# Performance work log

Hardware: AMD Instinct MI355X
Metric: run time of the kernel (lower is better)

Reference implementation:

```python
import jax, jax.numpy as jnp
import numpy as np
import math

PHI = (1 + math.sqrt(5)) / 2
VOCAB = 50257
EMBED_DIM = 1024
NUM_WINDINGS = 8
EPS = 1e-5


def _generate_coprimes(n):
    coprimes = [1, 2]
    while len(coprimes) < n:
        nxt = int(coprimes[-1] * PHI) + 1
        while any(math.gcd(nxt, c) > 1 for c in coprimes):
            nxt += 1
        coprimes.append(nxt)
    return coprimes[:n]


def setup_inputs() -> dict:
    key = jax.random.key(0)
    k1, k2, k3 = jax.random.split(key, 3)
    B, S = 8, 4096
    x = jax.random.randint(k1, (B, S), 0, VOCAB, dtype=jnp.int64)
    windings = jnp.asarray(_generate_coprimes(NUM_WINDINGS), dtype=jnp.float32)
    win_dim = 2 * NUM_WINDINGS
    # nn.Linear default init: U(-1/sqrt(fan_in), 1/sqrt(fan_in))
    bound = 1.0 / math.sqrt(win_dim)
    proj_w = jax.random.uniform(k2, (EMBED_DIM, win_dim), jnp.float32, -bound, bound)
    proj_b = jax.random.uniform(k3, (EMBED_DIM,), jnp.float32, -bound, bound)
    gamma = jnp.ones((EMBED_DIM,), jnp.float32)
    beta = jnp.zeros((EMBED_DIM,), jnp.float32)
    return {"x": x, "windings": windings, "proj_w": proj_w, "proj_b": proj_b,
            "gamma": gamma, "beta": beta}


def reference(x, windings, proj_w, proj_b, gamma, beta):
    # t in [0,1): fractional position on the torus
    t = x.astype(jnp.float32) / VOCAB                      # (B, S)
    angle = (2.0 * jnp.pi) * t[..., None] * windings       # (B, S, W)
    # torch loop appends cos, sin per winding -> interleaved [cos0,sin0,cos1,sin1,...]
    feats = jnp.stack([jnp.cos(angle), jnp.sin(angle)], axis=-1)  # (B, S, W, 2)
    feats = feats.reshape(*angle.shape[:-1], 2 * windings.shape[0])  # (B, S, 2W)
    emb = jnp.einsum('bsf,df->bsd', feats, proj_w) + proj_b  # (B, S, D)
    # SyntonicNorm: LayerNorm-style normalization over embed_dim with affine params
    mu = jnp.mean(emb, axis=-1, keepdims=True)
    var = jnp.mean(jnp.square(emb - mu), axis=-1, keepdims=True)
    normed = (emb - mu) * jax.lax.rsqrt(var + EPS)
    return normed * gamma + beta
```

## Files before the change

### kernel.cpp

```cpp
#include <hip/hip_runtime.h>
#include <math.h>


#define TWO_PI 6.28318530717958647692f
#define INV_VOCAB (1.0f / 50257.0f)
#define INV_D (1.0f / 1024.0f)
#define ROWS_PB 64
#define PSTRIDE 320
#define FINAL_OFF 20480

typedef float f32x4 __attribute__((ext_vector_type(4)));

__global__ __launch_bounds__(256) void stats_partial(const float* __restrict__ pw,
                                                     const float* __restrict__ pb,
                                                     float* __restrict__ ws) {
  const int t = threadIdx.x;
  const int b = blockIdx.x;
  const int f = t >> 4, g = t & 15;
  const int d0 = b * 16;

  float m = 0.f, mw = 0.f, cc = 0.f, b1 = 0.f, b2 = 0.f;
#pragma unroll
  for (int k = 0; k < 16; ++k) {
    const int d = d0 + k;
    const float wf = pw[d * 16 + f];
    const float wg = pw[d * 16 + g];
    m = fmaf(wf, wg, m);
    if (g == 0) {
      const float bb = pb[d];
      mw += wf;
      cc = fmaf(wf, bb, cc);
      if (f == 0) {
        b1 += bb;
        b2 = fmaf(bb, bb, b2);
      }
    }
  }
  float* p = ws + b * PSTRIDE;
  p[t] = m * INV_D;
  if (g == 0) {
    p[256 + f] = mw * INV_D;
    p[272 + f] = cc * INV_D;
    if (f == 0) {
      p[288] = b1 * INV_D;
      p[289] = b2 * INV_D;
    }
  }
}

__global__ __launch_bounds__(320) void stats_reduce(float* __restrict__ ws) {
  const int t = threadIdx.x;
  float s = 0.f;
#pragma unroll
  for (int b = 0; b < 64; ++b) s += ws[b * PSTRIDE + t];
  ws[FINAL_OFF + t] = s;
}

__global__ __launch_bounds__(256) void wind_main(const int* __restrict__ x,
                                                 const float* __restrict__ winds,
                                                 const float* __restrict__ pw,
                                                 const float* __restrict__ pb,
                                                 const float* __restrict__ gamma,
                                                 const float* __restrict__ beta,
                                                 const float* __restrict__ ws,
                                                 float* __restrict__ out) {
  __shared__ __align__(16) float feat[ROWS_PB][20];
  __shared__ __align__(16) float Mlds[16][20];
  __shared__ float mwl[16], cl[16], cst[2];
  __shared__ float murs[ROWS_PB][2];

  const int tid = threadIdx.x;
  const int row0 = blockIdx.x * ROWS_PB;

  Mlds[tid >> 4][tid & 15] = ws[FINAL_OFF + tid];
  if (tid < 16) mwl[tid] = ws[FINAL_OFF + 256 + tid];
  else if (tid < 32) cl[tid - 16] = ws[FINAL_OFF + 256 + tid];
  else if (tid < 34) cst[tid - 32] = ws[FINAL_OFF + 256 + tid];

  float4 wreg[4][4];
#pragma unroll
  for (int r = 0; r < 4; ++r)
#pragma unroll
    for (int c = 0; c < 4; ++c)
      wreg[r][c] = reinterpret_cast<const float4*>(pw)[(tid * 4 + r) * 4 + c];
  const float4 pbv = reinterpret_cast<const float4*>(pb)[tid];
  const float4 gv = reinterpret_cast<const float4*>(gamma)[tid];
  const float4 bv = reinterpret_cast<const float4*>(beta)[tid];

#pragma unroll
  for (int s = 0; s < 4; ++s) {
    const int slot = tid + s * 256;
    const int r = slot >> 4, jj = slot & 15;
    const float tf = (float)x[row0 + r] * INV_VOCAB;
    float sn, cs;
    sincosf(TWO_PI * tf * winds[jj >> 1], &sn, &cs);
    feat[r][jj] = (jj & 1) ? sn : cs;
  }
  __syncthreads();

  {
    const int jj = tid & 15;
    const float mwj = mwl[jj];
    const float cj = cl[jj];
    const f32x4 M0 = *reinterpret_cast<const f32x4*>(&Mlds[jj][0]);
    const f32x4 M1 = *reinterpret_cast<const f32x4*>(&Mlds[jj][4]);
    const f32x4 M2 = *reinterpret_cast<const f32x4*>(&Mlds[jj][8]);
    const f32x4 M3 = *reinterpret_cast<const f32x4*>(&Mlds[jj][12]);
#pragma unroll
    for (int h = 0; h < 4; ++h) {
      const int r = (tid >> 4) + h * 16;
      const f32x4 F0 = *reinterpret_cast<const f32x4*>(&feat[r][0]);
      const f32x4 F1 = *reinterpret_cast<const f32x4*>(&feat[r][4]);
      const f32x4 F2 = *reinterpret_cast<const f32x4*>(&feat[r][8]);
      const f32x4 F3 = *reinterpret_cast<const f32x4*>(&feat[r][12]);
      float acc = 0.f;
      acc = fmaf(M0.x, F0.x, acc); acc = fmaf(M0.y, F0.y, acc);
      acc = fmaf(M0.z, F0.z, acc); acc = fmaf(M0.w, F0.w, acc);
      acc = fmaf(M1.x, F1.x, acc); acc = fmaf(M1.y, F1.y, acc);
      acc = fmaf(M1.z, F1.z, acc); acc = fmaf(M1.w, F1.w, acc);
      acc = fmaf(M2.x, F2.x, acc); acc = fmaf(M2.y, F2.y, acc);
      acc = fmaf(M2.z, F2.z, acc); acc = fmaf(M2.w, F2.w, acc);
      acc = fmaf(M3.x, F3.x, acc); acc = fmaf(M3.y, F3.y, acc);
      acc = fmaf(M3.z, F3.z, acc); acc = fmaf(M3.w, F3.w, acc);
      const float fjj = feat[r][jj];
      float pE = fjj * fmaf(2.f, cj, acc);
      float pM = fjj * mwj;
#pragma unroll
      for (int off = 1; off < 16; off <<= 1) {
        pE += __shfl_xor(pE, off);
        pM += __shfl_xor(pM, off);
      }
      if (jj == 0) {
        const float mu = pM + cst[0];
        const float var = (pE + cst[1]) - mu * mu;
        murs[r][0] = mu;
        murs[r][1] = rsqrtf(var + 1e-5f);
      }
    }
  }
  __syncthreads();

  float* o = out + (size_t)row0 * 1024 + tid * 4;
#pragma unroll 2
  for (int r = 0; r < ROWS_PB; ++r) {
    const f32x4 F0 = *reinterpret_cast<const f32x4*>(&feat[r][0]);
    const f32x4 F1 = *reinterpret_cast<const f32x4*>(&feat[r][4]);
    const f32x4 F2 = *reinterpret_cast<const f32x4*>(&feat[r][8]);
    const f32x4 F3 = *reinterpret_cast<const f32x4*>(&feat[r][12]);
    float e[4];
#pragma unroll
    for (int k = 0; k < 4; ++k) {
      float a = (k == 0) ? pbv.x : (k == 1) ? pbv.y : (k == 2) ? pbv.z : pbv.w;
      a = fmaf(wreg[k][0].x, F0.x, a);
      a = fmaf(wreg[k][0].y, F0.y, a);
      a = fmaf(wreg[k][0].z, F0.z, a);
      a = fmaf(wreg[k][0].w, F0.w, a);
      a = fmaf(wreg[k][1].x, F1.x, a);
      a = fmaf(wreg[k][1].y, F1.y, a);
      a = fmaf(wreg[k][1].z, F1.z, a);
      a = fmaf(wreg[k][1].w, F1.w, a);
      a = fmaf(wreg[k][2].x, F2.x, a);
      a = fmaf(wreg[k][2].y, F2.y, a);
      a = fmaf(wreg[k][2].z, F2.z, a);
      a = fmaf(wreg[k][2].w, F2.w, a);
      a = fmaf(wreg[k][3].x, F3.x, a);
      a = fmaf(wreg[k][3].y, F3.y, a);
      a = fmaf(wreg[k][3].z, F3.z, a);
      a = fmaf(wreg[k][3].w, F3.w, a);
      e[k] = a;
    }
    const float mu = murs[r][0];
    const float rs = murs[r][1];
    const float s0 = gv.x * rs, s1 = gv.y * rs, s2 = gv.z * rs, s3 = gv.w * rs;
    f32x4 res;
    res.x = fmaf(e[0], s0, fmaf(-mu, s0, bv.x));
    res.y = fmaf(e[1], s1, fmaf(-mu, s1, bv.y));
    res.z = fmaf(e[2], s2, fmaf(-mu, s2, bv.z));
    res.w = fmaf(e[3], s3, fmaf(-mu, s3, bv.w));
    *reinterpret_cast<f32x4*>(o + (size_t)r * 1024) = res;
  }
}

extern "C" void kernel_launch(void* const* d_in, const int* in_sizes, int n_in,
                              void* d_out, int out_size, void* d_ws, size_t ws_size,
                              hipStream_t stream) {
  const int* x = (const int*)d_in[0];
  const float* winds = (const float*)d_in[1];
  const float* pw = (const float*)d_in[2];
  const float* pb = (const float*)d_in[3];
  const float* gamma = (const float*)d_in[4];
  const float* beta = (const float*)d_in[5];
  float* out = (float*)d_out;
  float* ws = (float*)d_ws;

  const int rows = in_sizes[0];
  stats_partial<<<64, 256, 0, stream>>>(pw, pb, ws);
  stats_reduce<<<1, 320, 0, stream>>>(ws);
  wind_main<<<rows / ROWS_PB, 256, 0, stream>>>(x, winds, pw, pb, gamma, beta,
                                                ws, out);
}
```

Measured before the change: 40.65 us.

## Fuse weight-statistics precompute into main kernel, recomputing per block

Removes the two separate statistics kernels (partial and reduce). Each block of the main kernel now recomputes the 16x16 Gram matrix of proj_w, the column sums, and the bias cross terms from its register-resident weights, using wave shuffle reductions and a small LDS combine. This removes two kernel launches and the serial dependency through the workspace. In exchange every block repeats redundant compute and many cross-lane shuffles (roughly 170 values x 6 shuffle steps per wave) before it writes any output.

```diff
diff --git a/kernel.cpp b/kernel.cpp
--- a/kernel.cpp
+++ b/kernel.cpp
@@ -6,76 +6,43 @@
 #define INV_VOCAB (1.0f / 50257.0f)
 #define INV_D (1.0f / 1024.0f)
 #define ROWS_PB 64
-#define PSTRIDE 320
-#define FINAL_OFF 20480
 
 typedef float f32x4 __attribute__((ext_vector_type(4)));
 
-__global__ __launch_bounds__(256) void stats_partial(const float* __restrict__ pw,
-                                                     const float* __restrict__ pb,
-                                                     float* __restrict__ ws) {
-  const int t = threadIdx.x;
-  const int b = blockIdx.x;
-  const int f = t >> 4, g = t & 15;
-  const int d0 = b * 16;
-
-  float m = 0.f, mw = 0.f, cc = 0.f, b1 = 0.f, b2 = 0.f;
-#pragma unroll
-  for (int k = 0; k < 16; ++k) {
-    const int d = d0 + k;
-    const float wf = pw[d * 16 + f];
-    const float wg = pw[d * 16 + g];
-    m = fmaf(wf, wg, m);
-    if (g == 0) {
-      const float bb = pb[d];
-      mw += wf;
-      cc = fmaf(wf, bb, cc);
-      if (f == 0) {
-        b1 += bb;
-        b2 = fmaf(bb, bb, b2);
-      }
-    }
-  }
-  float* p = ws + b * PSTRIDE;
-  p[t] = m * INV_D;
-  if (g == 0) {
-    p[256 + f] = mw * INV_D;
-    p[272 + f] = cc * INV_D;
-    if (f == 0) {
-      p[288] = b1 * INV_D;
-      p[289] = b2 * INV_D;
-    }
-  }
-}
-
-__global__ __launch_bounds__(320) void stats_reduce(float* __restrict__ ws) {
-  const int t = threadIdx.x;
-  float s = 0.f;
-#pragma unroll
-  for (int b = 0; b < 64; ++b) s += ws[b * PSTRIDE + t];
-  ws[FINAL_OFF + t] = s;
-}
-
-__global__ __launch_bounds__(256) void wind_main(const int* __restrict__ x,
-                                                 const float* __restrict__ winds,
-                                                 const float* __restrict__ pw,
-                                                 const float* __restrict__ pb,
-                                                 const float* __restrict__ gamma,
-                                                 const float* __restrict__ beta,
-                                                 const float* __restrict__ ws,
-                                                 float* __restrict__ out) {
+#define WEL(r, c)                                                          \
+  (((c) & 3) == 0   ? wreg[r][(c) >> 2].x                                  \
+   : ((c) & 3) == 1 ? wreg[r][(c) >> 2].y                                  \
+   : ((c) & 3) == 2 ? wreg[r][(c) >> 2].z                                  \
+                    : wreg[r][(c) >> 2].w)
+
+#define ME(s, j, i)                                                        \
+  acc[s] = fmaf(WEL(3, j), WEL(3, i),                                      \
+           fmaf(WEL(2, j), WEL(2, i),                                      \
+           fmaf(WEL(1, j), WEL(1, i), WEL(0, j) * WEL(0, i))));
+
+__global__ __launch_bounds__(256) void wind_one(const int* __restrict__ x,
+                                                const float* __restrict__ winds,
+                                                const float* __restrict__ pw,
+                                                const float* __restrict__ pb,
+                                                const float* __restrict__ gamma,
+                                                const float* __restrict__ beta,
+                                                float* __restrict__ out) {
   __shared__ __align__(16) float feat[ROWS_PB][20];
   __shared__ __align__(16) float Mlds[16][20];
+  __shared__ float Mwp[4][4][34];
+  __shared__ float Vwp[4][34];
   __shared__ float mwl[16], cl[16], cst[2];
   __shared__ float murs[ROWS_PB][2];
 
   const int tid = threadIdx.x;
+  const int wave = tid >> 6;
+  const int lane = tid & 63;
   const int row0 = blockIdx.x * ROWS_PB;
 
-  Mlds[tid >> 4][tid & 15] = ws[FINAL_OFF + tid];
-  if (tid < 16) mwl[tid] = ws[FINAL_OFF + 256 + tid];
-  else if (tid < 32) cl[tid - 16] = ws[FINAL_OFF + 256 + tid];
-  else if (tid < 34) cst[tid - 32] = ws[FINAL_OFF + 256 + tid];
+  float tfv[4];
+#pragma unroll
+  for (int s = 0; s < 4; ++s)
+    tfv[s] = (float)x[row0 + ((tid + s * 256) >> 4)] * INV_VOCAB;
 
   float4 wreg[4][4];
 #pragma unroll
@@ -87,14 +54,101 @@
   const float4 gv = reinterpret_cast<const float4*>(gamma)[tid];
   const float4 bv = reinterpret_cast<const float4*>(beta)[tid];
 
+  {
+    float v[34];
+#pragma unroll
+    for (int c = 0; c < 16; ++c) {
+      v[c] = (WEL(0, c) + WEL(1, c)) + (WEL(2, c) + WEL(3, c));
+      v[16 + c] = fmaf(WEL(0, c), pbv.x, fmaf(WEL(1, c), pbv.y,
+                  fmaf(WEL(2, c), pbv.z, WEL(3, c) * pbv.w)));
+    }
+    v[32] = (pbv.x + pbv.y) + (pbv.z + pbv.w);
+    v[33] = fmaf(pbv.x, pbv.x, fmaf(pbv.y, pbv.y, fmaf(pbv.z, pbv.z, pbv.w * pbv.w)));
+#pragma unroll
+    for (int s = 0; s < 34; ++s)
+#pragma unroll
+      for (int off = 1; off < 64; off <<= 1) v[s] += __shfl_xor(v[s], off);
+    if (lane == 0)
+#pragma unroll
+      for (int s = 0; s < 34; ++s) Vwp[wave][s] = v[s];
+  }
+
+#pragma unroll 1
+  for (int p = 0; p < 4; ++p) {
+    const int set = (wave + p) & 3;
+    float acc[34];
+    if (set == 0) {
+      ME(0,0,0) ME(1,0,1) ME(2,0,2) ME(3,0,3) ME(4,0,4) ME(5,0,5) ME(6,0,6)
+      ME(7,0,7) ME(8,0,8) ME(9,0,9) ME(10,0,10) ME(11,0,11) ME(12,0,12)
+      ME(13,0,13) ME(14,0,14) ME(15,0,15)
+      ME(16,1,1) ME(17,1,2) ME(18,1,3) ME(19,1,4) ME(20,1,5) ME(21,1,6)
+      ME(22,1,7) ME(23,1,8) ME(24,1,9) ME(25,1,10) ME(26,1,11) ME(27,1,12)
+      ME(28,1,13) ME(29,1,14) ME(30,1,15)
+      ME(31,2,2) ME(32,2,3) ME(33,2,4)
+    } else if (set == 1) {
+      ME(0,2,5) ME(1,2,6) ME(2,2,7) ME(3,2,8) ME(4,2,9) ME(5,2,10) ME(6,2,11)
+      ME(7,2,12) ME(8,2,13) ME(9,2,14) ME(10,2,15)
+      ME(11,3,3) ME(12,3,4) ME(13,3,5) ME(14,3,6) ME(15,3,7) ME(16,3,8)
+      ME(17,3,9) ME(18,3,10) ME(19,3,11) ME(20,3,12) ME(21,3,13) ME(22,3,14)
+      ME(23,3,15)
+      ME(24,4,4) ME(25,4,5) ME(26,4,6) ME(27,4,7) ME(28,4,8) ME(29,4,9)
+      ME(30,4,10) ME(31,4,11) ME(32,4,12) ME(33,4,13)
+    } else if (set == 2) {
+      ME(0,4,14) ME(1,4,15)
+      ME(2,5,5) ME(3,5,6) ME(4,5,7) ME(5,5,8) ME(6,5,9) ME(7,5,10) ME(8,5,11)
+      ME(9,5,12) ME(10,5,13) ME(11,5,14) ME(12,5,15)
+      ME(13,6,6) ME(14,6,7) ME(15,6,8) ME(16,6,9) ME(17,6,10) ME(18,6,11)
+      ME(19,6,12) ME(20,6,13) ME(21,6,14) ME(22,6,15)
+      ME(23,7,7) ME(24,7,8) ME(25,7,9) ME(26,7,10) ME(27,7,11) ME(28,7,12)
+      ME(29,7,13) ME(30,7,14) ME(31,7,15)
+      ME(32,8,8) ME(33,8,9)
+    } else {
+      ME(0,8,10) ME(1,8,11) ME(2,8,12) ME(3,8,13) ME(4,8,14) ME(5,8,15)
+      ME(6,9,9) ME(7,9,10) ME(8,9,11) ME(9,9,12) ME(10,9,13) ME(11,9,14)
+      ME(12,9,15)
+      ME(13,10,10) ME(14,10,11) ME(15,10,12) ME(16,10,13) ME(17,10,14)
+      ME(18,10,15)
+      ME(19,11,11) ME(20,11,12) ME(21,11,13) ME(22,11,14) ME(23,11,15)
+      ME(24,12,12) ME(25,12,13) ME(26,12,14) ME(27,12,15)
+      ME(28,13,13) ME(29,13,14) ME(30,13,15)
+      ME(31,14,14) ME(32,14,15)
+      ME(33,15,15)
+    }
+#pragma unroll
+    for (int s = 0; s < 34; ++s)
+#pragma unroll
+      for (int off = 1; off < 64; off <<= 1) acc[s] += __shfl_xor(acc[s], off);
+    if (lane == 0)
+#pragma unroll
+      for (int s = 0; s < 34; ++s) Mwp[set][wave][s] = acc[s];
+  }
+
 #pragma unroll
   for (int s = 0; s < 4; ++s) {
     const int slot = tid + s * 256;
     const int r = slot >> 4, jj = slot & 15;
-    const float tf = (float)x[row0 + r] * INV_VOCAB;
     float sn, cs;
-    sincosf(TWO_PI * tf * winds[jj >> 1], &sn, &cs);
+    sincosf(TWO_PI * tfv[s] * winds[jj >> 1], &sn, &cs);
     feat[r][jj] = (jj & 1) ? sn : cs;
+  }
+  __syncthreads();
+
+  if (tid < 136) {
+    const int set = tid / 34, sl = tid - set * 34;
+    const float val = ((Mwp[set][0][sl] + Mwp[set][1][sl]) +
+                       (Mwp[set][2][sl] + Mwp[set][3][sl])) * INV_D;
+    int e = tid, j = 0;
+    while (e >= 16 - j) { e -= 16 - j; ++j; }
+    const int i = j + e;
+    Mlds[j][i] = val;
+    Mlds[i][j] = val;
+  } else if (tid < 170) {
+    const int sl = tid - 136;
+    const float val = ((Vwp[0][sl] + Vwp[1][sl]) +
+                       (Vwp[2][sl] + Vwp[3][sl])) * INV_D;
+    if (sl < 16) mwl[sl] = val;
+    else if (sl < 32) cl[sl - 16] = val;
+    else cst[sl - 32] = val;
   }
   __syncthreads();
 
@@ -191,11 +245,7 @@
   const float* gamma = (const float*)d_in[4];
   const float* beta = (const float*)d_in[5];
   float* out = (float*)d_out;
-  float* ws = (float*)d_ws;
 
   const int rows = in_sizes[0];
-  stats_partial<<<64, 256, 0, stream>>>(pw, pb, ws);
-  stats_reduce<<<1, 320, 0, stream>>>(ws);
-  wind_main<<<rows / ROWS_PB, 256, 0, stream>>>(x, winds, pw, pb, gamma, beta,
-                                                ws, out);
+  wind_one<<<rows / ROWS_PB, 256, 0, stream>>>(x, winds, pw, pb, gamma, beta, out);
 }
```

New measurement: 61.29 us. 50.8% more time.
